# Kernel tuning notes

Hardware: AMD Instinct MI355X
Metric: run time of the kernel (lower is better)

Reference implementation:

```python
import jax, jax.numpy as jnp
import numpy as np

ATOMS = 51
V_MIN = -10.0
V_MAX = 10.0
GAMMA = 0.99
NSTEPS = 1
BATCH = 1048576
DELTA = (V_MAX - V_MIN) / (ATOMS - 1)


def setup_inputs() -> dict:
    key = jax.random.key(0)
    k1, k2, k3 = jax.random.split(key, 3)
    batch_reward = jax.random.normal(k1, (BATCH,), dtype=jnp.float32)
    # next-state distribution: positive and normalized over atoms (softmax-net output)
    raw = jax.random.uniform(k2, (BATCH, ATOMS), dtype=jnp.float32) + 1e-3
    max_next_dist = raw / raw.sum(axis=-1, keepdims=True)
    supports = jnp.linspace(V_MIN, V_MAX, ATOMS, dtype=jnp.float32)
    non_final_mask = jax.random.randint(k3, (BATCH,), 0, 2, dtype=jnp.int32)
    return {
        "batch_reward": batch_reward,
        "max_next_dist": max_next_dist,
        "supports": supports,
        "non_final_mask": non_final_mask,
    }


def reference(batch_reward, max_next_dist, supports, non_final_mask):
    B, A = max_next_dist.shape  # [B, atoms]
    mask_f = non_final_mask.astype(jnp.float32)
    # Tz = r + gamma^n * z * mask, clamped to [v_min, v_max]
    Tz = batch_reward[:, None] + (GAMMA ** NSTEPS) * supports[None, :] * mask_f[:, None]
    Tz = jnp.clip(Tz, V_MIN, V_MAX)
    b = (Tz - V_MIN) / DELTA                       # [B, A] float bin positions
    l = jnp.floor(b).astype(jnp.int32)
    u = jnp.ceil(b).astype(jnp.int32)
    # disambiguate exact-integer bins (sequential, matching torch in-place order)
    l = jnp.where((u > 0) & (l == u), l - 1, l)
    u = jnp.where((l < A - 1) & (l == u), u + 1, u)
    w_l = max_next_dist * (u.astype(jnp.float32) - b)   # weight to lower bin
    w_u = max_next_dist * (b - l.astype(jnp.float32))   # weight to upper bin
    offset = (jnp.arange(B, dtype=jnp.int32) * A)[:, None]  # [B, 1]
    m = jnp.zeros((B * A,), dtype=jnp.float32)
    m = m.at[(l + offset).ravel()].add(w_l.ravel())
    m = m.at[(u + offset).ravel()].add(w_u.ravel())
    return m.reshape(B, A)
```

## Files before the change

kernel.cpp:

```cpp
#include <hip/hip_runtime.h>


#define ATOMS 51
#define RPB   128
#define ELEMS (RPB * ATOMS)
#define VEC4  (ELEMS / 4)
#define VEC2  (ELEMS / 2)

__device__ __forceinline__ unsigned int f32_to_bf16_rn(float f) {
    unsigned int u = __builtin_bit_cast(unsigned int, f);
    u += 0x7fffu + ((u >> 16) & 1u);
    return u >> 16;
}
__device__ __forceinline__ float bf16_to_f32(unsigned short h) {
    return __builtin_bit_cast(float, (unsigned int)h << 16);
}

__global__ __launch_bounds__(RPB, 6) void c51_project(
    const float* __restrict__ reward,
    const float* __restrict__ dist,
    const float* __restrict__ supports,
    const int*   __restrict__ mask,
    float* __restrict__ out)
{
    __shared__ __align__(16) unsigned short tile[ELEMS];

    const int tid = threadIdx.x;
    const long long blk = blockIdx.x;
    const float4* __restrict__ src4 = (const float4*)(dist + blk * ELEMS);
    float2*       __restrict__ dst2 = (float2*)(out  + blk * ELEMS);

    float4 tmp[13];
    #pragma unroll
    for (int k = 0; k < 13; ++k) {
        int i = tid + k * RPB;
        if (i < VEC4) tmp[k] = src4[i];
    }
    #pragma unroll
    for (int k = 0; k < 13; ++k) {
        int i = tid + k * RPB;
        if (i < VEC4) {
            uint2 pk;
            pk.x = f32_to_bf16_rn(tmp[k].x) | (f32_to_bf16_rn(tmp[k].y) << 16);
            pk.y = f32_to_bf16_rn(tmp[k].z) | (f32_to_bf16_rn(tmp[k].w) << 16);
            ((uint2*)tile)[i] = pk;
        }
    }

    const int rowg = (int)blk * RPB + tid;
    const float r  = reward[rowg];
    const float mf = (float)mask[rowg];

    __syncthreads();

    const int base = tid * ATOMS;
    float p[ATOMS];
    #pragma unroll
    for (int j = 0; j < ATOMS; ++j) p[j] = bf16_to_f32(tile[base + j]);

    #pragma unroll
    for (int j = 0; j < ATOMS; ++j) tile[base + j] = 0;

    int cur; float accum, carry;
    {
        const float sz = 0.99f * supports[0];
        float Tz = r + sz * mf;
        Tz = fminf(fmaxf(Tz, -10.0f), 10.0f);
        float b = (Tz + 10.0f) * 2.5f;
        int l = (int)ceilf(b) - 1;
        l = (l < 0) ? 0 : l;
        float lf = (float)l;
        cur   = l;
        accum = p[0] * (lf + 1.0f - b);
        carry = p[0] * (b - lf);
    }
    #pragma unroll
    for (int j = 1; j < ATOMS; ++j) {
        const float sz = 0.99f * supports[j];
        float Tz = r + sz * mf;
        Tz = fminf(fmaxf(Tz, -10.0f), 10.0f);
        float b = (Tz + 10.0f) * 2.5f;
        int l = (int)ceilf(b) - 1;
        l = (l < 0) ? 0 : l;
        float lf = (float)l;
        float wl = p[j] * (lf + 1.0f - b);
        float wu = p[j] * (b - lf);
        if (l != cur) {
            tile[base + cur] = (unsigned short)f32_to_bf16_rn(accum);
            accum = carry;
            carry = 0.0f;
            cur = l;
        }
        accum += wl;
        carry += wu;
    }
    tile[base + cur]     = (unsigned short)f32_to_bf16_rn(accum);
    tile[base + cur + 1] = (unsigned short)f32_to_bf16_rn(carry);

    __syncthreads();

    #pragma unroll
    for (int k = 0; k < 26; ++k) {
        int i = tid + k * RPB;
        if (i < VEC2) {
            unsigned int pk = ((const unsigned int*)tile)[i];
            float2 o;
            o.x = bf16_to_f32((unsigned short)(pk & 0xffffu));
            o.y = bf16_to_f32((unsigned short)(pk >> 16));
            dst2[i] = o;
        }
    }
}

extern "C" void kernel_launch(void* const* d_in, const int* in_sizes, int n_in,
                              void* d_out, int out_size, void* d_ws, size_t ws_size,
                              hipStream_t stream) {
    const float* reward   = (const float*)d_in[0];
    const float* dist     = (const float*)d_in[1];
    const float* supports = (const float*)d_in[2];
    const int*   mask     = (const int*)d_in[3];
    float* out = (float*)d_out;
    const int B = in_sizes[0];
    const int grid = B / RPB;
    c51_project<<<grid, RPB, 0, stream>>>(reward, dist, supports, mask, out);
}
```

Before: 370.6 us.

## Double-buffer tiles with direct global-to-LDS loads in single-wave blocks

Replaces the one-tile-per-block kernel with 64-thread, single-wavefront blocks that each process four 64-row tiles. Tiles are double-buffered in LDS and filled with global_load_lds async copies, and the next tile is issued while the current one is computed. The bf16 staging is dropped, so LDS holds fp32, which removes the rounding error and the pack and unpack work but doubles LDS use. It relies on manual vmcnt/lgkmcnt waits instead of block barriers. That wait logic is fragile: vmcnt(13) must match the 15 loads issued per tile plus the reward and mask loads, and it is unclear whether the first tile's LDS data is fully waited on.

Result: no change. 375.9 us (+1.4%).

```diff
diff --git a/kernel.cpp b/kernel.cpp
--- a/kernel.cpp
+++ b/kernel.cpp
@@ -1,115 +1,107 @@
 #include <hip/hip_runtime.h>
 
 
-#define ATOMS 51
-#define RPB   128
-#define ELEMS (RPB * ATOMS)
-#define VEC4  (ELEMS / 4)
-#define VEC2  (ELEMS / 2)
+#define ATOMS   51
+#define ROWS    64
+#define TILE_F  (ROWS * ATOMS)
+#define TPB     4
 
-__device__ __forceinline__ unsigned int f32_to_bf16_rn(float f) {
-    unsigned int u = __builtin_bit_cast(unsigned int, f);
-    u += 0x7fffu + ((u >> 16) & 1u);
-    return u >> 16;
-}
-__device__ __forceinline__ float bf16_to_f32(unsigned short h) {
-    return __builtin_bit_cast(float, (unsigned int)h << 16);
-}
+#define WAIT_VM13()  asm volatile("s_waitcnt vmcnt(13)" ::: "memory")
+#define WAIT_LGKM0() asm volatile("s_waitcnt lgkmcnt(0)" ::: "memory")
+#define SCHED_FENCE() __builtin_amdgcn_sched_barrier(0)
 
-__global__ __launch_bounds__(RPB, 6) void c51_project(
+#define GLOAD_LDS16(g, l)                                                       \
+  __builtin_amdgcn_global_load_lds(                                             \
+      (const __attribute__((address_space(1))) void*)(g),                       \
+      (__attribute__((address_space(3))) void*)(l), 16, 0, 0)
+#define GLOAD_LDS4(g, l)                                                        \
+  __builtin_amdgcn_global_load_lds(                                             \
+      (const __attribute__((address_space(1))) void*)(g),                       \
+      (__attribute__((address_space(3))) void*)(l), 4, 0, 0)
+
+#define ISSUE_TILE(TT, S, RREG, MREG) do {                                      \
+    const int rowg_ = (TT) * ROWS + lane;                                       \
+    RREG = reward[rowg_];                                                       \
+    MREG = (float)mask[rowg_];                                                  \
+    const float* gsrc_ = dist + (size_t)(TT) * TILE_F;                          \
+    _Pragma("unroll")                                                           \
+    for (int k = 0; k < 12; ++k)                                                \
+      GLOAD_LDS16(gsrc_ + k * 256 + lane * 4, &smem[S][k * 256]);               \
+    _Pragma("unroll")                                                           \
+    for (int k = 0; k < 3; ++k)                                                 \
+      GLOAD_LDS4(gsrc_ + 3072 + k * 64 + lane, &smem[S][3072 + k * 64]);        \
+  } while (0)
+
+#define BODY(TIDX, S, RREG, MREG, DO_ISSUE) do {                                \
+    const int tt_ = tile0 + (TIDX);                                             \
+    WAIT_VM13();                             \
+    SCHED_FENCE();                            \
+    float* row = &smem[S][lane * ATOMS];                                        \
+    float p[ATOMS];                                                             \
+    _Pragma("unroll")                                                           \
+    for (int j = 0; j < ATOMS; ++j) p[j] = row[j];                              \
+    _Pragma("unroll")                                                           \
+    for (int j = 0; j < ATOMS; ++j) row[j] = 0.0f;                              \
+    const float r_  = RREG;                                                     \
+    const float mf_ = MREG;                                                     \
+    int cur_; float accum_, carry_;                                             \
+    {                                                                           \
+      float Tz = fminf(fmaxf(fmaf(0.99f * supports[0], mf_, r_), -10.0f), 10.0f); \
+      float b  = (Tz + 10.0f) * 2.5f;                                           \
+      int   l  = (int)ceilf(b) - 1;  l = (l < 0) ? 0 : l;                       \
+      float lf = (float)l;                                                      \
+      cur_   = l;                                                               \
+      accum_ = p[0] * (lf + 1.0f - b);                                          \
+      carry_ = p[0] * (b - lf);                                                 \
+    }                                                                           \
+    _Pragma("unroll")                                                           \
+    for (int j = 1; j < ATOMS; ++j) {                                           \
+      float Tz = fminf(fmaxf(fmaf(0.99f * supports[j], mf_, r_), -10.0f), 10.0f); \
+      float b  = (Tz + 10.0f) * 2.5f;                                           \
+      int   l  = (int)ceilf(b) - 1;  l = (l < 0) ? 0 : l;                       \
+      float lf = (float)l;                                                      \
+      float wl = p[j] * (lf + 1.0f - b);                                        \
+      float wu = p[j] * (b - lf);                                               \
+      if (l != cur_) {                    \
+        row[cur_] = accum_;                                                     \
+        accum_ = carry_; carry_ = 0.0f; cur_ = l;                               \
+      }                                                                         \
+      accum_ += wl; carry_ += wu;                                               \
+    }                                                                           \
+    row[cur_]     = accum_;                                                     \
+    row[cur_ + 1] = carry_;                              \
+             \
+    float4* dst4 = (float4*)(out + (size_t)tt_ * TILE_F);                       \
+    const float4* src4 = (const float4*)&smem[S][0];                            \
+    _Pragma("unroll")                                                           \
+    for (int k = 0; k < 12; ++k) dst4[lane + 64 * k] = src4[lane + 64 * k];     \
+    if (lane < 48) dst4[lane + 768] = src4[lane + 768];                         \
+    if (DO_ISSUE) {                                                             \
+      WAIT_LGKM0();                    \
+      SCHED_FENCE();                                                            \
+      ISSUE_TILE(tt_ + 2, S, RREG, MREG);                                       \
+    }                                                                           \
+  } while (0)
+
+__global__ __launch_bounds__(ROWS, 1) void c51_project(
     const float* __restrict__ reward,
     const float* __restrict__ dist,
     const float* __restrict__ supports,
     const int*   __restrict__ mask,
     float* __restrict__ out)
 {
-    __shared__ __align__(16) unsigned short tile[ELEMS];
+    __shared__ __align__(16) float smem[2][TILE_F];
+    const int lane  = threadIdx.x;
+    const int tile0 = blockIdx.x * TPB;
 
-    const int tid = threadIdx.x;
-    const long long blk = blockIdx.x;
-    const float4* __restrict__ src4 = (const float4*)(dist + blk * ELEMS);
-    float2*       __restrict__ dst2 = (float2*)(out  + blk * ELEMS);
+    float r0, m0, r1, m1;
+    ISSUE_TILE(tile0 + 0, 0, r0, m0);
+    ISSUE_TILE(tile0 + 1, 1, r1, m1);
 
-    float4 tmp[13];
-    #pragma unroll
-    for (int k = 0; k < 13; ++k) {
-        int i = tid + k * RPB;
-        if (i < VEC4) tmp[k] = src4[i];
-    }
-    #pragma unroll
-    for (int k = 0; k < 13; ++k) {
-        int i = tid + k * RPB;
-        if (i < VEC4) {
-            uint2 pk;
-            pk.x = f32_to_bf16_rn(tmp[k].x) | (f32_to_bf16_rn(tmp[k].y) << 16);
-            pk.y = f32_to_bf16_rn(tmp[k].z) | (f32_to_bf16_rn(tmp[k].w) << 16);
-            ((uint2*)tile)[i] = pk;
-        }
-    }
-
-    const int rowg = (int)blk * RPB + tid;
-    const float r  = reward[rowg];
-    const float mf = (float)mask[rowg];
-
-    __syncthreads();
-
-    const int base = tid * ATOMS;
-    float p[ATOMS];
-    #pragma unroll
-    for (int j = 0; j < ATOMS; ++j) p[j] = bf16_to_f32(tile[base + j]);
-
-    #pragma unroll
-    for (int j = 0; j < ATOMS; ++j) tile[base + j] = 0;
-
-    int cur; float accum, carry;
-    {
-        const float sz = 0.99f * supports[0];
-        float Tz = r + sz * mf;
-        Tz = fminf(fmaxf(Tz, -10.0f), 10.0f);
-        float b = (Tz + 10.0f) * 2.5f;
-        int l = (int)ceilf(b) - 1;
-        l = (l < 0) ? 0 : l;
-        float lf = (float)l;
-        cur   = l;
-        accum = p[0] * (lf + 1.0f - b);
-        carry = p[0] * (b - lf);
-    }
-    #pragma unroll
-    for (int j = 1; j < ATOMS; ++j) {
-        const float sz = 0.99f * supports[j];
-        float Tz = r + sz * mf;
-        Tz = fminf(fmaxf(Tz, -10.0f), 10.0f);
-        float b = (Tz + 10.0f) * 2.5f;
-        int l = (int)ceilf(b) - 1;
-        l = (l < 0) ? 0 : l;
-        float lf = (float)l;
-        float wl = p[j] * (lf + 1.0f - b);
-        float wu = p[j] * (b - lf);
-        if (l != cur) {
-            tile[base + cur] = (unsigned short)f32_to_bf16_rn(accum);
-            accum = carry;
-            carry = 0.0f;
-            cur = l;
-        }
-        accum += wl;
-        carry += wu;
-    }
-    tile[base + cur]     = (unsigned short)f32_to_bf16_rn(accum);
-    tile[base + cur + 1] = (unsigned short)f32_to_bf16_rn(carry);
-
-    __syncthreads();
-
-    #pragma unroll
-    for (int k = 0; k < 26; ++k) {
-        int i = tid + k * RPB;
-        if (i < VEC2) {
-            unsigned int pk = ((const unsigned int*)tile)[i];
-            float2 o;
-            o.x = bf16_to_f32((unsigned short)(pk & 0xffffu));
-            o.y = bf16_to_f32((unsigned short)(pk >> 16));
-            dst2[i] = o;
-        }
-    }
+    BODY(0, 0, r0, m0, true);
+    BODY(1, 1, r1, m1, true);
+    BODY(2, 0, r0, m0, false);
+    BODY(3, 1, r1, m1, false);
 }
 
 extern "C" void kernel_launch(void* const* d_in, const int* in_sizes, int n_in,
@@ -120,7 +112,8 @@
     const float* supports = (const float*)d_in[2];
     const int*   mask     = (const int*)d_in[3];
     float* out = (float*)d_out;
-    const int B = in_sizes[0];
-    const int grid = B / RPB;
-    c51_project<<<grid, RPB, 0, stream>>>(reward, dist, supports, mask, out);
+    const int B     = in_sizes[0];
+    const int tiles = B / ROWS;
+    const int grid  = tiles / TPB;
+    c51_project<<<grid, ROWS, 0, stream>>>(reward, dist, supports, mask, out);
 }
```
